# Kernel tuning notes

Measured on AMD Instinct MI355X. Metric: run time of the kernel, lower is better.

Reference implementation:

```python
import jax, jax.numpy as jnp
import numpy as np


def setup_inputs() -> dict:
    key = jax.random.key(0)
    k1, k2 = jax.random.split(key)
    B, T, D = 16, 512, 256
    feats = jax.random.normal(k1, (B, T, D), dtype=jnp.float32)
    hidden = jax.random.normal(k2, (B, T, 2 * D), dtype=jnp.float32)
    return {"feats": feats, "hidden": hidden, "seq_len": T}


def reference(feats, hidden, seq_len):
    # feats: (B, T, D); hidden: (B, T, 2D); all sequences have length seq_len == T
    B, T, D = feats.shape
    zero = jnp.zeros((B, 1, D), dtype=feats.dtype)
    # X_fw layout per sequence: [feat_0..feat_{T-1}, 0]; X_bw: [0, feat_0..feat_{T-1}]
    X_fw = jnp.concatenate([feats, zero], axis=1).reshape(B * (T + 1), D)
    X_bw = jnp.concatenate([zero, feats], axis=1).reshape(B * (T + 1), D)

    h_fw = hidden[..., :D]  # (B, T, D) forward LSTM half
    h_bw = hidden[..., D:]  # (B, T, D) backward LSTM half

    # (B, T, N) with N = B*(T+1): full softmax over every token slot (as original)
    fw_lp = jax.nn.log_softmax(jnp.einsum('btd,nd->btn', h_fw, X_fw), axis=-1)
    bw_lp = jax.nn.log_softmax(jnp.einsum('btd,nd->btn', h_bw, X_bw), axis=-1)

    t = jnp.arange(T)
    # original takes diag of columns [1:1+T] (fw) and [0:T] (bw) for EVERY sequence
    fw_diag = fw_lp[:, t, t + 1]  # (B, T)
    bw_diag = bw_lp[:, t, t]      # (B, T)

    fw_loss = (-fw_diag.sum(axis=1) / seq_len).sum() / B
    bw_loss = (-bw_diag.sum(axis=1) / seq_len).sum() / B
    return fw_loss, bw_loss
```

## Files before the change

### kernel.cpp

```cpp
#include <hip/hip_runtime.h>
#include <hip/hip_bf16.h>
#include <stdint.h>

typedef int int32x4 __attribute__((ext_vector_type(4)));

#define D      256
#define TLEN   512
#define BATCH  16
#define NQ     16384
#define NK     8192
#define KS     16
#define SLICE_KEYS (NK / KS)
#define BN     16
#define NT     (SLICE_KEYS / BN)
#define TILE_B (BN * D)
#define MSHIFT 64.0f
#define QSCALE 32.0f
#define SSCALE  11818.5577749f
#define SMAGIC2 290554713.0f

__device__ __forceinline__ int q8(float x) {
    float y = x * QSCALE;
    y = fminf(fmaxf(y, -127.f), 127.f);
    return (int)rintf(y);
}

__device__ __forceinline__ void quant16(const float* __restrict__ src,
                                        int32x4* __restrict__ dst, int i) {
    const float4* s4 = reinterpret_cast<const float4*>(src) + (size_t)i * 4;
    int32x4 o;
    #pragma unroll
    for (int j = 0; j < 4; ++j) {
        float4 v = s4[j];
        o[j] = (q8(v.x) & 255) | ((q8(v.y) & 255) << 8) |
               ((q8(v.z) & 255) << 16) | ((q8(v.w) & 255) << 24);
    }
    dst[i] = o;
}

__global__ void prep_kernel(const float* __restrict__ feats,
                            const float* __restrict__ hidden,
                            int32x4* __restrict__ Qi8, int32x4* __restrict__ Ki8,
                            float* __restrict__ tfw, float* __restrict__ tbw) {
    int b = blockIdx.x;
    if (b < 1024) {
        quant16(hidden, Qi8, b * 256 + threadIdx.x);
        return;
    }
    if (b < 1536) {
        quant16(feats, Ki8, (b - 1024) * 256 + threadIdx.x);
        return;
    }
    int gw   = (b - 1536) * 4 + (threadIdx.x >> 6);
    int lane = threadIdx.x & 63;
    int t = gw & (TLEN - 1);
    const float4* h4 = reinterpret_cast<const float4*>(hidden + (size_t)gw * (2 * D));
    float sfw = 0.f, sbw = 0.f;
    if (t < TLEN - 1) {
        const float4* f4 = reinterpret_cast<const float4*>(feats + (size_t)(t + 1) * D);
        float4 x = h4[lane], y = f4[lane];
        sfw = x.x * y.x + x.y * y.y + x.z * y.z + x.w * y.w;
    }
    if (t > 0) {
        const float4* f4 = reinterpret_cast<const float4*>(feats + (size_t)(t - 1) * D);
        float4 x = h4[64 + lane], y = f4[lane];
        sbw = x.x * y.x + x.y * y.y + x.z * y.z + x.w * y.w;
    }
    #pragma unroll
    for (int mask = 32; mask > 0; mask >>= 1) {
        sfw += __shfl_xor(sfw, mask);
        sbw += __shfl_xor(sbw, mask);
    }
    if (lane == 0) { tfw[gw] = sfw; tbw[gw] = sbw; }
}

__global__ __launch_bounds__(256, 2) void lse_kernel(const char* __restrict__ Qi8,
                                                     const char* __restrict__ Ki8,
                                                     float* __restrict__ ps) {
    const int bid   = (int)blockIdx.x;
    const int nbid  = (bid & 7) * 128 + (bid >> 3);
    const int slice = nbid >> 6;
    const int qblk  = nbid & 63;
    const int q0    = qblk * 256;
    const int wave  = (int)(threadIdx.x >> 6);
    const int lane  = (int)(threadIdx.x & 63);
    const int lrow  = lane & 15;
    const int lgrp  = lane >> 4;

    __shared__ __align__(16) char lds[4][2][TILE_B];
    char* myl = &lds[wave][0][0];

    int32x4 a[4][4];
    #pragma unroll
    for (int mf = 0; mf < 4; ++mf) {
        const char* qbase = Qi8 + (size_t)(q0 + wave * 64 + mf * 16 + lrow) * D + lgrp * 16;
        #pragma unroll
        for (int s = 0; s < 4; ++s)
            a[mf][s] = *reinterpret_cast<const int32x4*>(qbase + s * 64);
    }

    int voff[4];
    #pragma unroll
    for (int s = 0; s < 4; ++s)
        voff[s] = lrow * 256 + (((s * 4 + lgrp) ^ (lrow & 7)) * 16);

    int soff[4];
    #pragma unroll
    for (int i = 0; i < 4; ++i) {
        int cl  = lane + i * 64;
        int row = cl >> 4, c = cl & 15;
        soff[i] = (row * 16 + (c ^ (row & 7))) * 16;
    }

    const char* ksrc = Ki8 + (size_t)slice * (SLICE_KEYS * D);

    auto issue = [&](int buf, int t) {
        const char* tb = ksrc + (size_t)t * TILE_B;
        #pragma unroll
        for (int i = 0; i < 4; ++i) {
            const char* gp = tb + soff[i];
            char* lp = myl + buf * TILE_B + i * 1024;
            __builtin_amdgcn_global_load_lds(
                (const __attribute__((address_space(1))) void*)gp,
                (__attribute__((address_space(3))) void*)lp,
                16, 0, 0);
        }
    };

    float srun[4][4];
    #pragma unroll
    for (int mf = 0; mf < 4; ++mf)
        #pragma unroll
        for (int r = 0; r < 4; ++r) srun[mf][r] = 0.f;

    issue(0, 0);
    issue(1, 1);

    #pragma unroll 1
    for (int t = 0; t < NT; ++t) {
        if (t < NT - 1) asm volatile("s_waitcnt vmcnt(4)" ::: "memory");
        else            asm volatile("s_waitcnt vmcnt(0)" ::: "memory");

        const char* kb = myl + (t & 1) * TILE_B;
        int32x4 c[4];
        #pragma unroll
        for (int mf = 0; mf < 4; ++mf) c[mf] = (int32x4){0, 0, 0, 0};
        __builtin_amdgcn_s_setprio(1);
        #pragma unroll
        for (int s = 0; s < 4; ++s) {
            int32x4 b = *reinterpret_cast<const int32x4*>(kb + voff[s]);
            #pragma unroll
            for (int mf = 0; mf < 4; ++mf)
                c[mf] = __builtin_amdgcn_mfma_i32_16x16x64_i8(a[mf][s], b, c[mf], 0, 0, 0);
        }
        __builtin_amdgcn_s_setprio(0);
        asm volatile("" ::: "memory");
        if (t + 2 < NT) issue(t & 1, t + 2);

        #pragma unroll
        for (int mf = 0; mf < 4; ++mf)
            #pragma unroll
            for (int r = 0; r < 4; ++r) {
                float f = (float)c[mf][r];
                float tt = fmaxf(fmaf(f, SSCALE, SMAGIC2), 0.f);
                srun[mf][r] += __uint_as_float((uint32_t)tt);
            }
    }

    #pragma unroll
    for (int mf = 0; mf < 4; ++mf)
        #pragma unroll
        for (int r = 0; r < 4; ++r) {
            float v = srun[mf][r];
            v += __shfl_xor(v, 1);
            v += __shfl_xor(v, 2);
            v += __shfl_xor(v, 4);
            v += __shfl_xor(v, 8);
            if (lrow == 0) {
                int q = q0 + wave * 64 + mf * 16 + lgrp * 4 + r;
                ps[slice * NQ + q] = v;
            }
        }
}

__global__ void reduce1_kernel(const float* __restrict__ ps,
                               const float* __restrict__ tfw, const float* __restrict__ tbw,
                               float* __restrict__ partial) {
    __shared__ float red0[256], red1[256];
    int tid = threadIdx.x;
    int i   = blockIdx.x * 256 + tid;
    const float Z16 = 16.f * __expf(-MSHIFT);
    int qf = 2 * i, qb = 2 * i + 1;
    float sfw = Z16, sbw = Z16;
    #pragma unroll
    for (int sl = 0; sl < KS; ++sl) {
        sfw += ps[sl * NQ + qf];
        sbw += ps[sl * NQ + qb];
    }
    float lsef = MSHIFT + logf(sfw);
    float lseb = MSHIFT + logf(sbw);
    red0[tid] = lsef - tfw[i];
    red1[tid] = lseb - tbw[i];
    __syncthreads();
    for (int s2 = 128; s2 > 0; s2 >>= 1) {
        if (tid < s2) { red0[tid] += red0[tid + s2]; red1[tid] += red1[tid + s2]; }
        __syncthreads();
    }
    if (tid == 0) {
        partial[blockIdx.x * 2 + 0] = red0[0];
        partial[blockIdx.x * 2 + 1] = red1[0];
    }
}

__global__ void reduce2_kernel(const float* __restrict__ partial, float* __restrict__ out) {
    int lane = threadIdx.x & 63;
    float fw = (lane < 32) ? partial[lane * 2 + 0] : 0.f;
    float bw = (lane < 32) ? partial[lane * 2 + 1] : 0.f;
    #pragma unroll
    for (int mask = 32; mask > 0; mask >>= 1) {
        fw += __shfl_xor(fw, mask);
        bw += __shfl_xor(bw, mask);
    }
    if (lane == 0) {
        const float denom = (float)TLEN * (float)BATCH;
        out[0] = fw / denom;
        out[1] = bw / denom;
    }
}

extern "C" void kernel_launch(void* const* d_in, const int* in_sizes, int n_in,
                              void* d_out, int out_size, void* d_ws, size_t ws_size,
                              hipStream_t stream) {
    const float* feats  = (const float*)d_in[0];
    const float* hidden = (const float*)d_in[1];
    float* out = (float*)d_out;

    char* ws = (char*)d_ws;
    char*  Qi8  = ws;
    char*  Ki8  = ws + (size_t)NQ * D;
    float* psv  = (float*)(ws + (size_t)NQ * D + (size_t)NK * D);
    float* tfw  = psv + (size_t)KS * NQ;
    float* tbw  = tfw + NK;
    float* part = tbw + NK;

    prep_kernel<<<3584, 256, 0, stream>>>(feats, hidden,
                                          (int32x4*)Qi8, (int32x4*)Ki8, tfw, tbw);

    lse_kernel<<<(NQ / 256) * KS, 256, 0, stream>>>(Qi8, Ki8, psv);

    reduce1_kernel<<<NK / 256, 256, 0, stream>>>(psv, tfw, tbw, part);
    reduce2_kernel<<<1, 64, 0, stream>>>(part, out);
}
```

Baseline: 63.93 us.

## Switch to 32x32x32 int8 MFMA with software-pipelined exp accumulation

Replaces the 16x16x64 int8 MFMA tiling with 32x32x32 MFMAs over 32-key tiles, doubling the per-stage key tile and reworking the LDS swizzle and offsets to match. The main loop is unrolled by two with ping-pong accumulators, so the exp-approximation accumulation of one tile overlaps the MFMAs of the next. The clamp-to-zero is replaced by a saturating v_cvt_u32_f32 inline asm. This aims to raise MFMA throughput and hide the VALU epilogue, at the cost of more registers for the 16-wide accumulators and larger LDS buffers.

Result: slower. 73.02 us (+14.2%).

```diff
diff --git a/kernel.cpp b/kernel.cpp
--- a/kernel.cpp
+++ b/kernel.cpp
@@ -2,7 +2,8 @@
 #include <hip/hip_bf16.h>
 #include <stdint.h>
 
-typedef int int32x4 __attribute__((ext_vector_type(4)));
+typedef int int32x4  __attribute__((ext_vector_type(4)));
+typedef int int32x16 __attribute__((ext_vector_type(16)));
 
 #define D      256
 #define TLEN   512
@@ -11,13 +12,15 @@
 #define NK     8192
 #define KS     16
 #define SLICE_KEYS (NK / KS)
-#define BN     16
+#define BN     32
 #define NT     (SLICE_KEYS / BN)
 #define TILE_B (BN * D)
 #define MSHIFT 64.0f
 #define QSCALE 32.0f
 #define SSCALE  11818.5577749f
 #define SMAGIC2 290554713.0f
+
+#define VZERO16 (int32x16){0,0,0,0,0,0,0,0,0,0,0,0,0,0,0,0}
 
 __device__ __forceinline__ int q8(float x) {
     float y = x * QSCALE;
@@ -72,6 +75,17 @@
         sbw += __shfl_xor(sbw, mask);
     }
     if (lane == 0) { tfw[gw] = sfw; tbw[gw] = sbw; }
+}
+
+__device__ __forceinline__ void expacc(const int32x16& c, float (&sr)[16]) {
+    #pragma unroll
+    for (int r = 0; r < 16; ++r) {
+        float f  = (float)c[r];
+        float tt = fmaf(f, SSCALE, SMAGIC2);
+        uint32_t u;
+        asm("v_cvt_u32_f32 %0, %1" : "=v"(u) : "v"(tt));
+        sr[r] += __uint_as_float(u);
+    }
 }
 
 __global__ __launch_bounds__(256, 2) void lse_kernel(const char* __restrict__ Qi8,
@@ -84,32 +98,32 @@
     const int q0    = qblk * 256;
     const int wave  = (int)(threadIdx.x >> 6);
     const int lane  = (int)(threadIdx.x & 63);
-    const int lrow  = lane & 15;
-    const int lgrp  = lane >> 4;
+    const int row   = lane & 31;
+    const int hi    = lane >> 5;
 
     __shared__ __align__(16) char lds[4][2][TILE_B];
     char* myl = &lds[wave][0][0];
 
-    int32x4 a[4][4];
-    #pragma unroll
-    for (int mf = 0; mf < 4; ++mf) {
-        const char* qbase = Qi8 + (size_t)(q0 + wave * 64 + mf * 16 + lrow) * D + lgrp * 16;
-        #pragma unroll
-        for (int s = 0; s < 4; ++s)
-            a[mf][s] = *reinterpret_cast<const int32x4*>(qbase + s * 64);
-    }
-
-    int voff[4];
-    #pragma unroll
-    for (int s = 0; s < 4; ++s)
-        voff[s] = lrow * 256 + (((s * 4 + lgrp) ^ (lrow & 7)) * 16);
-
-    int soff[4];
-    #pragma unroll
-    for (int i = 0; i < 4; ++i) {
-        int cl  = lane + i * 64;
-        int row = cl >> 4, c = cl & 15;
-        soff[i] = (row * 16 + (c ^ (row & 7))) * 16;
+    int32x4 a[2][8];
+    #pragma unroll
+    for (int mf = 0; mf < 2; ++mf) {
+        const char* qbase = Qi8 + (size_t)(q0 + wave * 64 + mf * 32 + row) * D + hi * 16;
+        #pragma unroll
+        for (int s = 0; s < 8; ++s)
+            a[mf][s] = *reinterpret_cast<const int32x4*>(qbase + s * 32);
+    }
+
+    int voff[8];
+    #pragma unroll
+    for (int s = 0; s < 8; ++s)
+        voff[s] = row * 256 + (((s * 2 + hi) ^ (row & 7)) * 16);
+
+    int soff[8];
+    #pragma unroll
+    for (int i = 0; i < 8; ++i) {
+        int cl = lane + i * 64;
+        int rr = cl >> 4, cc = cl & 15;
+        soff[i] = (rr * 16 + (cc ^ (rr & 7))) * 16;
     }
 
     const char* ksrc = Ki8 + (size_t)slice * (SLICE_KEYS * D);
@@ -117,7 +131,7 @@
     auto issue = [&](int buf, int t) {
         const char* tb = ksrc + (size_t)t * TILE_B;
         #pragma unroll
-        for (int i = 0; i < 4; ++i) {
+        for (int i = 0; i < 8; ++i) {
             const char* gp = tb + soff[i];
             char* lp = myl + buf * TILE_B + i * 1024;
             __builtin_amdgcn_global_load_lds(
@@ -127,57 +141,63 @@
         }
     };
 
-    float srun[4][4];
-    #pragma unroll
-    for (int mf = 0; mf < 4; ++mf)
-        #pragma unroll
-        for (int r = 0; r < 4; ++r) srun[mf][r] = 0.f;
+    auto mfma_tile = [&](const char* kb, int32x16& c0, int32x16& c1) {
+        __builtin_amdgcn_s_setprio(1);
+        #pragma unroll
+        for (int s = 0; s < 8; ++s) {
+            int32x4 b = *reinterpret_cast<const int32x4*>(kb + voff[s]);
+            c0 = __builtin_amdgcn_mfma_i32_32x32x32_i8(a[0][s], b, c0, 0, 0, 0);
+            c1 = __builtin_amdgcn_mfma_i32_32x32x32_i8(a[1][s], b, c1, 0, 0, 0);
+        }
+        __builtin_amdgcn_s_setprio(0);
+    };
+
+    float srun[2][16];
+    #pragma unroll
+    for (int mf = 0; mf < 2; ++mf)
+        #pragma unroll
+        for (int r = 0; r < 16; ++r) srun[mf][r] = 0.f;
 
     issue(0, 0);
     issue(1, 1);
 
+    asm volatile("s_waitcnt vmcnt(8)" ::: "memory");
+    int32x16 cA0 = VZERO16, cA1 = VZERO16, cB0, cB1;
+    mfma_tile(myl, cA0, cA1);
+    issue(0, 2);
+
     #pragma unroll 1
-    for (int t = 0; t < NT; ++t) {
-        if (t < NT - 1) asm volatile("s_waitcnt vmcnt(4)" ::: "memory");
-        else            asm volatile("s_waitcnt vmcnt(0)" ::: "memory");
-
-        const char* kb = myl + (t & 1) * TILE_B;
-        int32x4 c[4];
-        #pragma unroll
-        for (int mf = 0; mf < 4; ++mf) c[mf] = (int32x4){0, 0, 0, 0};
-        __builtin_amdgcn_s_setprio(1);
-        #pragma unroll
-        for (int s = 0; s < 4; ++s) {
-            int32x4 b = *reinterpret_cast<const int32x4*>(kb + voff[s]);
-            #pragma unroll
-            for (int mf = 0; mf < 4; ++mf)
-                c[mf] = __builtin_amdgcn_mfma_i32_16x16x64_i8(a[mf][s], b, c[mf], 0, 0, 0);
-        }
-        __builtin_amdgcn_s_setprio(0);
-        asm volatile("" ::: "memory");
-        if (t + 2 < NT) issue(t & 1, t + 2);
-
-        #pragma unroll
-        for (int mf = 0; mf < 4; ++mf)
-            #pragma unroll
-            for (int r = 0; r < 4; ++r) {
-                float f = (float)c[mf][r];
-                float tt = fmaxf(fmaf(f, SSCALE, SMAGIC2), 0.f);
-                srun[mf][r] += __uint_as_float((uint32_t)tt);
-            }
-    }
-
-    #pragma unroll
-    for (int mf = 0; mf < 4; ++mf)
-        #pragma unroll
-        for (int r = 0; r < 4; ++r) {
+    for (int p = 0; p < NT / 2 - 1; ++p) {
+        asm volatile("s_waitcnt vmcnt(8)" ::: "memory");
+        cB0 = VZERO16; cB1 = VZERO16;
+        mfma_tile(myl + TILE_B, cB0, cB1);
+        issue(1, 2 * p + 3);
+        expacc(cA0, srun[0]); expacc(cA1, srun[1]);
+        asm volatile("s_waitcnt vmcnt(8)" ::: "memory");
+        cA0 = VZERO16; cA1 = VZERO16;
+        mfma_tile(myl, cA0, cA1);
+        if (p < NT / 2 - 2) issue(0, 2 * p + 4);
+        expacc(cB0, srun[0]); expacc(cB1, srun[1]);
+    }
+
+    asm volatile("s_waitcnt vmcnt(0)" ::: "memory");
+    cB0 = VZERO16; cB1 = VZERO16;
+    mfma_tile(myl + TILE_B, cB0, cB1);
+    expacc(cA0, srun[0]); expacc(cA1, srun[1]);
+    expacc(cB0, srun[0]); expacc(cB1, srun[1]);
+
+    #pragma unroll
+    for (int mf = 0; mf < 2; ++mf)
+        #pragma unroll
+        for (int r = 0; r < 16; ++r) {
             float v = srun[mf][r];
             v += __shfl_xor(v, 1);
             v += __shfl_xor(v, 2);
             v += __shfl_xor(v, 4);
             v += __shfl_xor(v, 8);
-            if (lrow == 0) {
-                int q = q0 + wave * 64 + mf * 16 + lgrp * 4 + r;
+            v += __shfl_xor(v, 16);
+            if ((lane & 31) == 0) {
+                int q = q0 + wave * 64 + mf * 32 + (r & 3) + 8 * (r >> 2) + 4 * hi;
                 ps[slice * NQ + q] = v;
             }
         }
```
